# Kernel tuning notes

Measured on AMD Instinct MI355X. Metric: run time of the kernel, lower is better.

## Reference

```python
import jax, jax.numpy as jnp
import numpy as np

EPS = 1e-8  # torch CosineSimilarity default eps


def setup_inputs() -> dict:
    key = jax.random.key(0)
    k_emb, k_idx, k_w1, k_w2 = jax.random.split(key, 4)
    N, H, E = 50000, 128, 800000
    emb = jax.random.normal(k_emb, (N, H), dtype=jnp.float32)
    edge_index = jax.random.randint(k_idx, (2, E), 0, N, dtype=jnp.int64)
    # xavier_uniform for square H x H: limit = sqrt(6 / (H + H))
    lim = float(np.sqrt(6.0 / (H + H)))
    W1 = jax.random.uniform(k_w1, (H, H), dtype=jnp.float32, minval=-lim, maxval=lim)
    W2 = jax.random.uniform(k_w2, (H, H), dtype=jnp.float32, minval=-lim, maxval=lim)
    b1 = jnp.zeros((H,), dtype=jnp.float32)
    b2 = jnp.zeros((H,), dtype=jnp.float32)
    return {"emb": emb, "edge_index": edge_index, "W1": W1, "b1": b1, "W2": W2, "b2": b2}


def reference(emb, edge_index, W1, b1, W2, b2):
    col, row = edge_index[0], edge_index[1]

    def mlp(x):  # Linear -> (Dropout: identity at eval) -> ELU -> Linear
        h = jax.nn.elu(x @ W1.T + b1)
        return h @ W2.T + b2

    f1 = mlp(emb[col])  # [E, H]
    f2 = mlp(emb[row])  # [E, H]
    n1 = jnp.maximum(jnp.sqrt(jnp.sum(f1 * f1, axis=1)), EPS)
    n2 = jnp.maximum(jnp.sqrt(jnp.sum(f2 * f2, axis=1)), EPS)
    return jnp.sum(f1 * f2, axis=1) / (n1 * n2)  # [E]
```

## Files before the change

### kernel.cpp

```cpp
#include <hip/hip_runtime.h>
#include <math.h>

#define H 128
#define XS 136

#if defined(__has_builtin)
# if __has_builtin(__builtin_amdgcn_sdot4)
#  define HAVE_SDOT4 1
# endif
#endif

typedef __attribute__((ext_vector_type(8))) short short8;
typedef __attribute__((ext_vector_type(4))) float floatx4;
typedef __attribute__((ext_vector_type(4))) int intx4;

__device__ __forceinline__ unsigned short f2bf(float f) {
    unsigned u = __float_as_uint(f);
    return (unsigned short)((u + 0x7FFFu + ((u >> 16) & 1u)) >> 16);
}

__global__ void prep_weights(const float* __restrict__ W1,
                             const float* __restrict__ W2,
                             unsigned short* __restrict__ Wbf) {
    int i = blockIdx.x * 256 + threadIdx.x;
    if (i < 16384)       Wbf[i] = f2bf(W1[i]);
    else if (i < 32768)  Wbf[i] = f2bf(W2[i - 16384]);
}

__global__ __launch_bounds__(64, 4) void mlp_wave(
    const float* __restrict__ emb, const unsigned short* __restrict__ Wbf,
    const float* __restrict__ b1, const float* __restrict__ b2,
    signed char* __restrict__ qtab, float* __restrict__ scl, int N)
{
    __shared__ unsigned short hs[16 * XS];

    const int lane  = threadIdx.x;
    const int quad  = lane >> 4, l15 = lane & 15;
    const int node0 = blockIdx.x * 16;
    const int grow  = node0 + l15;
    const bool rv   = grow < N;

    short8 afr[4];
    #pragma unroll
    for (int ks = 0; ks < 4; ++ks) {
        float4 u0 = make_float4(0.f, 0.f, 0.f, 0.f);
        float4 u1 = make_float4(0.f, 0.f, 0.f, 0.f);
        if (rv) {
            const float* p = emb + (size_t)grow * H + ks * 32 + quad * 8;
            u0 = *(const float4*)p;
            u1 = *(const float4*)(p + 4);
        }
        short8 a;
        a[0] = (short)f2bf(u0.x); a[1] = (short)f2bf(u0.y);
        a[2] = (short)f2bf(u0.z); a[3] = (short)f2bf(u0.w);
        a[4] = (short)f2bf(u1.x); a[5] = (short)f2bf(u1.y);
        a[6] = (short)f2bf(u1.z); a[7] = (short)f2bf(u1.w);
        afr[ks] = a;
    }

    #pragma unroll
    for (int nt = 0; nt < 8; ++nt) {
        floatx4 acc = {0.f, 0.f, 0.f, 0.f};
        #pragma unroll
        for (int ks = 0; ks < 4; ++ks) {
            short8 bfr = *(const short8*)(Wbf + (nt * 16 + l15) * H + ks * 32 + quad * 8);
            acc = __builtin_amdgcn_mfma_f32_16x16x32_bf16(afr[ks], bfr, acc, 0, 0, 0);
        }
        const int col = nt * 16 + l15;
        const float bb1 = b1[col];
        #pragma unroll
        for (int r = 0; r < 4; ++r) {
            float v = acc[r] + bb1;
            v = v > 0.f ? v : (__expf(v) - 1.f);
            hs[(quad * 4 + r) * XS + col] = f2bf(v);
        }
    }
    __syncthreads();

    #pragma unroll
    for (int ks = 0; ks < 4; ++ks)
        afr[ks] = *(const short8*)(hs + l15 * XS + ks * 32 + quad * 8);

    floatx4 av[8];
    float sq[4] = {0.f, 0.f, 0.f, 0.f};
    float am[4] = {0.f, 0.f, 0.f, 0.f};
    #pragma unroll
    for (int nt = 0; nt < 8; ++nt) {
        floatx4 acc = {0.f, 0.f, 0.f, 0.f};
        #pragma unroll
        for (int ks = 0; ks < 4; ++ks) {
            short8 bfr = *(const short8*)(Wbf + 16384 + (nt * 16 + l15) * H + ks * 32 + quad * 8);
            acc = __builtin_amdgcn_mfma_f32_16x16x32_bf16(afr[ks], bfr, acc, 0, 0, 0);
        }
        const float bb2 = b2[nt * 16 + l15];
        #pragma unroll
        for (int r = 0; r < 4; ++r) {
            float v = acc[r] + bb2;
            av[nt][r] = v;
            sq[r] += v * v;
            am[r] = fmaxf(am[r], fabsf(v));
        }
    }
    #pragma unroll
    for (int r = 0; r < 4; ++r) {
        float s = sq[r], a = am[r];
        #pragma unroll
        for (int m = 8; m; m >>= 1) {
            s += __shfl_xor(s, m);
            a = fmaxf(a, __shfl_xor(a, m));
        }
        sq[r] = s; am[r] = a;
    }
    #pragma unroll
    for (int r = 0; r < 4; ++r) {
        const int row = quad * 4 + r;
        const int G = node0 + row;
        if (G < N) {
            const float a = fmaxf(am[r], 1e-20f);
            if (l15 == 0) {
                float nn = sqrtf(sq[r]);
                if (nn < 1e-8f) nn = 1e-8f;
                scl[G] = a / (nn * 127.f);
            }
            const float qs = 127.f / a;
            unsigned pk0 = 0, pk1 = 0;
            #pragma unroll
            for (int nt = 0; nt < 4; ++nt) {
                int q = (int)rintf(av[nt][r] * qs);
                q = q > 127 ? 127 : (q < -127 ? -127 : q);
                pk0 |= ((unsigned)(q & 255)) << (8 * nt);
            }
            #pragma unroll
            for (int nt = 4; nt < 8; ++nt) {
                int q = (int)rintf(av[nt][r] * qs);
                q = q > 127 ? 127 : (q < -127 ? -127 : q);
                pk1 |= ((unsigned)(q & 255)) << (8 * (nt - 4));
            }
            *(uint2*)(qtab + (size_t)G * H + l15 * 8) = make_uint2(pk0, pk1);
        }
    }
}

__device__ __forceinline__ int dot4s(unsigned a, unsigned b) {
    int s = 0;
    #pragma unroll
    for (int j = 0; j < 4; ++j)
        s += (int)((signed char)(a >> (8 * j))) * (int)((signed char)(b >> (8 * j)));
    return s;
}

__device__ __forceinline__ int dot16(uint4 a, uint4 b) {
#if defined(HAVE_SDOT4)
    int s = __builtin_amdgcn_sdot4((int)a.x, (int)b.x, 0, false);
    s = __builtin_amdgcn_sdot4((int)a.y, (int)b.y, s, false);
    s = __builtin_amdgcn_sdot4((int)a.z, (int)b.z, s, false);
    s = __builtin_amdgcn_sdot4((int)a.w, (int)b.w, s, false);
    return s;
#else
    return dot4s(a.x, b.x) + dot4s(a.y, b.y) + dot4s(a.z, b.z) + dot4s(a.w, b.w);
#endif
}

__global__ __launch_bounds__(256) void edge_cos(
    const int* __restrict__ ei, const signed char* __restrict__ qtab,
    const float* __restrict__ scl, float* __restrict__ out, int E)
{
    const int tid = threadIdx.x;
    const int sub = tid & 7;
    const int g   = (blockIdx.x * 256 + tid) >> 3;
    const int e0  = g * 4;
    if (e0 >= E) return;

    int cc[4], rr[4];
    if (e0 + 3 < E) {
        intx4 c4 = __builtin_nontemporal_load((const intx4*)(ei + e0));
        intx4 r4 = __builtin_nontemporal_load((const intx4*)(ei + E + e0));
        cc[0] = c4.x; cc[1] = c4.y; cc[2] = c4.z; cc[3] = c4.w;
        rr[0] = r4.x; rr[1] = r4.y; rr[2] = r4.z; rr[3] = r4.w;
    } else {
        #pragma unroll
        for (int k = 0; k < 4; ++k) {
            int e = e0 + k; if (e >= E) e = E - 1;
            cc[k] = __builtin_nontemporal_load(ei + e);
            rr[k] = __builtin_nontemporal_load(ei + e + E);
        }
    }
    uint4 ua[4], ub[4];
    #pragma unroll
    for (int k = 0; k < 4; ++k) {
        ua[k] = *(const uint4*)(qtab + (size_t)cc[k] * H + sub * 16);
        ub[k] = *(const uint4*)(qtab + (size_t)rr[k] * H + sub * 16);
    }
    float sc[4];
    #pragma unroll
    for (int k = 0; k < 4; ++k) sc[k] = scl[cc[k]] * scl[rr[k]];

    #pragma unroll
    for (int k = 0; k < 4; ++k) {
        int s = dot16(ua[k], ub[k]);
        s += __shfl_xor(s, 4);
        s += __shfl_xor(s, 2);
        s += __shfl_xor(s, 1);
        if (sub == 0 && e0 + k < E)
            __builtin_nontemporal_store((float)s * sc[k], out + e0 + k);
    }
}

extern "C" void kernel_launch(void* const* d_in, const int* in_sizes, int n_in,
                              void* d_out, int out_size, void* d_ws, size_t ws_size,
                              hipStream_t stream) {
    const float* emb = (const float*)d_in[0];
    const int*   ei  = (const int*)d_in[1];
    const float* W1  = (const float*)d_in[2];
    const float* b1  = (const float*)d_in[3];
    const float* W2  = (const float*)d_in[4];
    const float* b2  = (const float*)d_in[5];
    float*       out = (float*)d_out;

    const int N = in_sizes[0] / H;
    const int E = in_sizes[1] / 2;

    unsigned short* Wbf  = (unsigned short*)d_ws;
    signed char*    qtab = (signed char*)(Wbf + 32768);
    float*          sclp = (float*)(qtab + (size_t)N * H);

    prep_weights<<<128, 256, 0, stream>>>(W1, W2, Wbf);
    mlp_wave<<<(N + 15) / 16, 64, 0, stream>>>(emb, Wbf, b1, b2, qtab, sclp, N);
    edge_cos<<<(E + 127) / 128, 256, 0, stream>>>(ei, qtab, sclp, out, E);
}
```

Measured before the change: 133.3 us.

## Stage MLP weights in LDS across 4-wave blocks; dedupe edge scale loads via shuffles

The node MLP kernel now runs 256-thread blocks of 64 nodes and copies each bf16 weight matrix into padded LDS once per block. The waves then read their MFMA B fragments from LDS instead of each wave re-reading the weights from global memory. This adds two extra barriers and about 52KB of LDS per block, which may limit occupancy. The edge kernel changes its scale lookups so each lane loads one scale value per edge endpoint, then shares the products with shuffles instead of having all 8 sub-lanes redundantly gather scl values.

```diff
diff --git a/kernel.cpp b/kernel.cpp
--- a/kernel.cpp
+++ b/kernel.cpp
@@ -2,6 +2,7 @@
 #include <math.h>
 
 #define H 128
+#define MROWS 64
 #define XS 136
 
 #if defined(__has_builtin)
@@ -27,18 +28,32 @@
     else if (i < 32768)  Wbf[i] = f2bf(W2[i - 16384]);
 }
 
-__global__ __launch_bounds__(64, 4) void mlp_wave(
+__global__ __launch_bounds__(256, 3) void mlp_mfma(
     const float* __restrict__ emb, const unsigned short* __restrict__ Wbf,
     const float* __restrict__ b1, const float* __restrict__ b2,
     signed char* __restrict__ qtab, float* __restrict__ scl, int N)
 {
-    __shared__ unsigned short hs[16 * XS];
-
-    const int lane  = threadIdx.x;
+    __shared__ unsigned short Wl[H * XS];
+    __shared__ unsigned short hs[MROWS * XS];
+
+    const int tid   = threadIdx.x;
+    const int wave  = tid >> 6, lane = tid & 63;
     const int quad  = lane >> 4, l15 = lane & 15;
-    const int node0 = blockIdx.x * 16;
-    const int grow  = node0 + l15;
+    const int node0 = blockIdx.x * MROWS;
+
+    const int  mrow = wave * 16 + l15;
+    const int  grow = node0 + mrow;
     const bool rv   = grow < N;
+
+    {
+        const float4* src = (const float4*)Wbf;
+        #pragma unroll
+        for (int i = 0; i < 8; ++i) {
+            int cc = i * 256 + tid;
+            int row = cc >> 4, c = cc & 15;
+            *(float4*)(Wl + row * XS + c * 8) = src[cc];
+        }
+    }
 
     short8 afr[4];
     #pragma unroll
@@ -57,13 +72,14 @@
         a[6] = (short)f2bf(u1.z); a[7] = (short)f2bf(u1.w);
         afr[ks] = a;
     }
+    __syncthreads();
 
     #pragma unroll
     for (int nt = 0; nt < 8; ++nt) {
         floatx4 acc = {0.f, 0.f, 0.f, 0.f};
         #pragma unroll
         for (int ks = 0; ks < 4; ++ks) {
-            short8 bfr = *(const short8*)(Wbf + (nt * 16 + l15) * H + ks * 32 + quad * 8);
+            short8 bfr = *(const short8*)(Wl + (nt * 16 + l15) * XS + ks * 32 + quad * 8);
             acc = __builtin_amdgcn_mfma_f32_16x16x32_bf16(afr[ks], bfr, acc, 0, 0, 0);
         }
         const int col = nt * 16 + l15;
@@ -72,14 +88,24 @@
         for (int r = 0; r < 4; ++r) {
             float v = acc[r] + bb1;
             v = v > 0.f ? v : (__expf(v) - 1.f);
-            hs[(quad * 4 + r) * XS + col] = f2bf(v);
+            hs[(wave * 16 + quad * 4 + r) * XS + col] = f2bf(v);
         }
     }
     __syncthreads();
 
     #pragma unroll
     for (int ks = 0; ks < 4; ++ks)
-        afr[ks] = *(const short8*)(hs + l15 * XS + ks * 32 + quad * 8);
+        afr[ks] = *(const short8*)(hs + mrow * XS + ks * 32 + quad * 8);
+    {
+        const float4* src = (const float4*)(Wbf + 16384);
+        #pragma unroll
+        for (int i = 0; i < 8; ++i) {
+            int cc = i * 256 + tid;
+            int row = cc >> 4, c = cc & 15;
+            *(float4*)(Wl + row * XS + c * 8) = src[cc];
+        }
+    }
+    __syncthreads();
 
     floatx4 av[8];
     float sq[4] = {0.f, 0.f, 0.f, 0.f};
@@ -89,7 +115,7 @@
         floatx4 acc = {0.f, 0.f, 0.f, 0.f};
         #pragma unroll
         for (int ks = 0; ks < 4; ++ks) {
-            short8 bfr = *(const short8*)(Wbf + 16384 + (nt * 16 + l15) * H + ks * 32 + quad * 8);
+            short8 bfr = *(const short8*)(Wl + (nt * 16 + l15) * XS + ks * 32 + quad * 8);
             acc = __builtin_amdgcn_mfma_f32_16x16x32_bf16(afr[ks], bfr, acc, 0, 0, 0);
         }
         const float bb2 = b2[nt * 16 + l15];
@@ -113,7 +139,7 @@
     }
     #pragma unroll
     for (int r = 0; r < 4; ++r) {
-        const int row = quad * 4 + r;
+        const int row = wave * 16 + quad * 4 + r;
         const int G = node0 + row;
         if (G < N) {
             const float a = fmaxf(am[r], 1e-20f);
@@ -165,10 +191,24 @@
     const int* __restrict__ ei, const signed char* __restrict__ qtab,
     const float* __restrict__ scl, float* __restrict__ out, int E)
 {
-    const int tid = threadIdx.x;
-    const int sub = tid & 7;
-    const int g   = (blockIdx.x * 256 + tid) >> 3;
-    const int e0  = g * 4;
+    const int tid   = threadIdx.x;
+    const int wlane = tid & 63;
+    const int sub   = tid & 7;
+    const int grp   = wlane >> 3;
+    const int g     = (blockIdx.x * 256 + tid) >> 3;
+    const int e0    = g * 4;
+
+    const int wbase = ((blockIdx.x * 256 + (tid & ~63)) >> 3) * 4;
+
+    float my_s = 0.f;
+    {
+        int el = wbase + (wlane & 31);
+        if (el >= E) el = E - 1;
+        const int idx = (wlane < 32) ? el : el + E;
+        my_s = scl[__builtin_nontemporal_load(ei + idx)];
+    }
+    const float prod = my_s * __shfl_xor(my_s, 32);
+
     if (e0 >= E) return;
 
     int cc[4], rr[4];
@@ -193,7 +233,7 @@
     }
     float sc[4];
     #pragma unroll
-    for (int k = 0; k < 4; ++k) sc[k] = scl[cc[k]] * scl[rr[k]];
+    for (int k = 0; k < 4; ++k) sc[k] = __shfl(prod, grp * 4 + k);
 
     #pragma unroll
     for (int k = 0; k < 4; ++k) {
@@ -225,6 +265,7 @@
     float*          sclp = (float*)(qtab + (size_t)N * H);
 
     prep_weights<<<128, 256, 0, stream>>>(W1, W2, Wbf);
-    mlp_wave<<<(N + 15) / 16, 64, 0, stream>>>(emb, Wbf, b1, b2, qtab, sclp, N);
+    mlp_mfma<<<(N + MROWS - 1) / MROWS, 256, 0, stream>>>(emb, Wbf, b1, b2,
+                                                          qtab, sclp, N);
     edge_cos<<<(E + 127) / 128, 256, 0, stream>>>(ei, qtab, sclp, out, E);
 }
```

Measured after the change: 120.0 us. -10.0%, faster.
